# Optimization experiments

Measured on AMD Instinct MI355X. Metric: run time of the kernel, lower is better.

The kernel has to match this reference:

```python
import jax, jax.numpy as jnp
import numpy as np

N_TH1 = 30
LB = 1e-20
UB = 1e20
LB_EXP = -20.0
UB_EXP = 20.0


def make_directions(n_th1):
    # Reproduces the TF __init__ direction sampling on the sphere.
    n_th2 = 2 * (n_th1 - 1) + 1
    th1 = np.linspace(-np.pi / 2, np.pi / 2, n_th1)
    th2 = np.linspace(-np.pi, np.pi, n_th2)
    c1, s1 = np.cos(th1), np.sin(th1)
    c2, s2 = np.cos(th2), np.sin(th2)
    dx = np.outer(c1[1:-1], c2[:-1])          # [n_th1-2, n_th2-1]
    dy = np.outer(c1[1:-1], s2[:-1])
    dz = np.broadcast_to(s1[1:-1, None], dx.shape)
    mid = np.stack([dx, dy, dz], -1).reshape(-1, 3)
    poles = np.array([[c1[0] * c2[0], c1[0] * s2[0], s1[0]],
                      [c1[-1] * c2[0], c1[-1] * s2[0], s1[-1]]])
    return np.concatenate([mid, poles], 0).astype(np.float32)  # [D, 3]


def setup_inputs() -> dict:
    key = jax.random.key(0)
    k1, k2, k3 = jax.random.split(key, 3)
    vertices = jax.random.normal(k1, (8, 64, 32, 3), jnp.float32)
    # smoothness is a p-norm exponent; realistic range [2, 20]
    smoothness = 2.0 + 18.0 * jax.random.uniform(k2, (8, 64), jnp.float32)
    pointcloud = jax.random.normal(k3, (8, 2048, 3), jnp.float32)
    return {"vertices": vertices, "smoothness": smoothness, "pointcloud": pointcloud}


def _spt_forward(vertices, smoothness):
    dirs = jnp.asarray(make_directions(N_TH1))            # [D, 3]
    B, P = vertices.shape[0], vertices.shape[1]
    mean_v = jnp.mean(vertices, axis=2, keepdims=True)    # [B,P,1,3]
    local_v = vertices - mean_v                           # [B,P,V,3]

    # z = <v, x> for every vertex/direction pair -> [B,P,V,D]
    z = jnp.einsum('bpvc,dc->bpvd', local_v, dirs)
    zm = jnp.maximum(z, 0.0)
    p = smoothness[:, :, None, None]                      # [B,P,1,1]

    # dynamic rescaling k = 10^ceil(...) to keep zm^p in fp range
    zm_max = jnp.max(zm, axis=2, keepdims=True)           # [B,P,1,D]
    zm_log = jnp.log(zm_max) / jnp.log(10.0)              # = max over V of log10(zm)
    exponent = zm_log * p
    lk = jnp.where(exponent < LB_EXP, (-15.0 - exponent) / p, 0.0)
    k = 10.0 ** jnp.clip(jnp.ceil(lk), 0.0, UB_EXP)       # [B,P,1,D]
    k = jax.lax.stop_gradient(k)                          # ceil has zero grad anyway

    zm = zm * k
    pos = zm > 0
    # clip(zm^p, lb, ub) - (zm==0)*lb  ==  where(zm>0, clip(zm^p,lb,ub), 0)
    zm_p = jnp.where(pos, jnp.clip(jnp.where(pos, zm, 1.0) ** p, LB, UB), 0.0)
    sum_zm_p = jnp.sum(zm_p, axis=2, keepdims=True)       # [B,P,1,D]
    spos = sum_zm_p > 0
    h = jnp.where(spos, jnp.clip(jnp.where(spos, sum_zm_p, 1.0) ** (1.0 / p), LB, UB), LB)

    # dh/dz = clip((zm/h)^(p-1), lb, ub)
    ratio = zm / h                                        # [B,P,V,D]
    rpos = ratio > 0
    dhdz = jnp.where(rpos, jnp.clip(jnp.where(rpos, ratio, 1.0) ** (p - 1.0), LB, UB), LB)
    # dh/dx = dhdz^T @ vertices -> surface points
    dhdx = jnp.einsum('bpvd,bpvc->bpdc', dhdz, local_v)   # [B,P,D,3]
    surf = dhdx + mean_v                                  # broadcast [B,P,1,3]

    h_out = jnp.clip(h / k, -UB, UB)                      # [B,P,1,D]
    h_out = jnp.transpose(h_out, (0, 1, 3, 2))            # [B,P,D,1]
    local_dirs = jnp.broadcast_to(dirs[None, None], (B, P) + dirs.shape)
    direction_h = jnp.concatenate([local_dirs, h_out], axis=-1)  # [B,P,D,4]
    points = surf.reshape(B, -1, 3)                       # [B, P*D, 3]
    mean_out = mean_v.reshape(B, P, 3)
    return points, direction_h, mean_out, local_v


def reference(vertices, smoothness, pointcloud):
    points, direction_h, mean_out, local_v = _spt_forward(vertices, smoothness)
    B, P = vertices.shape[0], vertices.shape[1]
    # overlap / retraction loops are truncated in the source; placeholders
    overlap = jnp.zeros((B, P, 1), jnp.float32)
    retraction = jnp.zeros((B, P, 1), jnp.float32)
    return (points, direction_h, overlap, retraction, mean_out, local_v)
```

## Files before the change

### kernel.cpp

```cpp
#include <hip/hip_runtime.h>
#include <math.h>

#define NBP 512
#define VV 32
#define DD 1626
#define DSPAN 407

#define O_POINTS 0
#define O_DIRH   2497536
#define O_OVER   5827584
#define O_RETR   5828096
#define O_MEAN   5828608
#define O_LOCAL  5830144

#define L10_2 0.3010299956639812f
#define L2_10 3.321928094887362f
#define LH_MIN -66.43856189774725f

__device__ __forceinline__ float fexp2(float x) {
  return __builtin_amdgcn_exp2f(x);
}

__device__ __forceinline__ void make_dir_fast(int d, float& x, float& y, float& z) {
  if (d < 1624) {
    const int i1 = d / 58 + 1;
    const int i2 = d - (i1 - 1) * 58;
    const float STEP = 0.10833078115826873f;
    const float th1 = -1.5707963267948966f + (float)i1 * STEP;
    const float th2 = -3.14159265358979323846f + (float)i2 * STEP;
    const float s1 = __sinf(th1);
    const float c1 = __cosf(th1);
    const float s2 = __sinf(th2);
    const float c2 = __cosf(th2);
    x = c1 * c2; y = c1 * s2; z = s1;
  } else if (d == 1624) {
    x = -6.123234e-17f; y = -7.49880e-33f; z = -1.0f;
  } else {
    x = -6.123234e-17f; y = -7.49880e-33f; z = 1.0f;
  }
}

__global__ __launch_bounds__(256) void spt_kernel(
    const float* __restrict__ vertices,
    const float* __restrict__ smooth,
    float* __restrict__ out)
{
  const int bp  = blockIdx.x;
  const int bz  = blockIdx.y;
  const int tid = threadIdx.x;

  __shared__ __align__(16) float slvx[VV];
  __shared__ __align__(16) float slvy[VV];
  __shared__ __align__(16) float slvz[VV];

  const int dbase = bz * DSPAN;
  const int dend  = (DD - dbase) < DSPAN ? (DD - dbase) : DSPAN;

  const int v = tid & 31;
  const float* vp = vertices + bp * (VV * 3) + v * 3;
  const float vx = vp[0], vy = vp[1], vz = vp[2];
  float sx = vx, sy = vy, sz = vz;
#pragma unroll
  for (int m = 16; m >= 1; m >>= 1) {
    sx += __shfl_xor(sx, m);
    sy += __shfl_xor(sy, m);
    sz += __shfl_xor(sz, m);
  }
  const float mx = sx * (1.0f / 32.0f);
  const float my = sy * (1.0f / 32.0f);
  const float mz = sz * (1.0f / 32.0f);
  if (tid < VV) {
    slvx[tid] = vx - mx;
    slvy[tid] = vy - my;
    slvz[tid] = vz - mz;
  }
  __syncthreads();

  if (bz == 1) {
    if (tid < VV * 3) {
      const int vv = tid / 3, c = tid - vv * 3;
      const float val = (c == 0) ? slvx[vv] : ((c == 1) ? slvy[vv] : slvz[vv]);
      out[O_LOCAL + bp * (VV * 3) + tid] = val;
    }
    if (tid == 96) {
      out[O_MEAN + bp * 3 + 0] = mx;
      out[O_MEAN + bp * 3 + 1] = my;
      out[O_MEAN + bp * 3 + 2] = mz;
      out[O_OVER + bp] = 0.f;
      out[O_RETR + bp] = 0.f;
    }
  }

  const float p     = smooth[bp];
  const float inv_p = 1.0f / p;
  const float pm1   = p - 1.0f;
  const float plt   = p * L10_2;

  const float4* lvx4 = (const float4*)slvx;
  const float4* lvy4 = (const float4*)slvy;
  const float4* lvz4 = (const float4*)slvz;

  auto process = [&](int idx) {
    const int d = dbase + idx;
    float dx, dy, dz;
    make_dir_fast(d, dx, dy, dz);

    float zmax = 0.f;
#pragma unroll
    for (int j = 0; j < VV / 4; j++) {
      float4 X = lvx4[j], Y = lvy4[j], Z = lvz4[j];
      float z0 = fmaxf(fmaf(X.x, dx, fmaf(Y.x, dy, Z.x * dz)), 0.f);
      float z1 = fmaxf(fmaf(X.y, dx, fmaf(Y.y, dy, Z.y * dz)), 0.f);
      float z2 = fmaxf(fmaf(X.z, dx, fmaf(Y.z, dy, Z.z * dz)), 0.f);
      float z3 = fmaxf(fmaf(X.w, dx, fmaf(Y.w, dy, Z.w * dz)), 0.f);
      zmax = fmaxf(zmax, fmaxf(fmaxf(z0, z1), fmaxf(z2, z3)));
    }

    const float expo = __log2f(zmax) * plt;
    float kc = 0.f;
    if (expo < -20.f) {
      kc = fminf(fmaxf(ceilf((-15.f - expo) * inv_p), 0.f), 20.f);
    }
    const float kcl = kc * L2_10;
    const float A   = p * kcl;

    float ss0 = 0.f, ss1 = 0.f;
    float ax = 0.f, ay = 0.f, az = 0.f;
#pragma unroll
    for (int j = 0; j < VV / 4; j++) {
      float4 X = lvx4[j], Y = lvy4[j], Z = lvz4[j];
      float z0 = fmaxf(fmaf(X.x, dx, fmaf(Y.x, dy, Z.x * dz)), 0.f);
      float z1 = fmaxf(fmaf(X.y, dx, fmaf(Y.y, dy, Z.y * dz)), 0.f);
      float z2 = fmaxf(fmaf(X.z, dx, fmaf(Y.z, dy, Z.z * dz)), 0.f);
      float z3 = fmaxf(fmaf(X.w, dx, fmaf(Y.w, dy, Z.w * dz)), 0.f);
      float u0 = fexp2(fmaf(pm1, __log2f(z0), A));
      float u1 = fexp2(fmaf(pm1, __log2f(z1), A));
      float u2 = fexp2(fmaf(pm1, __log2f(z2), A));
      float u3 = fexp2(fmaf(pm1, __log2f(z3), A));
      ss0 = fmaf(u0, z0, ss0);  ss1 = fmaf(u1, z1, ss1);
      ss0 = fmaf(u2, z2, ss0);  ss1 = fmaf(u3, z3, ss1);
      ax = fmaf(u0, X.x, fmaf(u1, X.y, fmaf(u2, X.z, fmaf(u3, X.w, ax))));
      ay = fmaf(u0, Y.x, fmaf(u1, Y.y, fmaf(u2, Y.z, fmaf(u3, Y.w, ay))));
      az = fmaf(u0, Z.x, fmaf(u1, Z.y, fmaf(u2, Z.z, fmaf(u3, Z.w, az))));
    }
    const float ssum = ss0 + ss1;

    float lh = LH_MIN;
    float C2 = 0.f;
    if (ssum > 0.f) {
      lh = inv_p * __log2f(ssum);
      C2 = fexp2(-fmaf(pm1, lh, kcl));
    }

    const int pbase = bp * DD + d;
    out[O_POINTS + pbase * 3 + 0] = fmaf(C2, ax, mx);
    out[O_POINTS + pbase * 3 + 1] = fmaf(C2, ay, my);
    out[O_POINTS + pbase * 3 + 2] = fmaf(C2, az, mz);

    float4 dvh = make_float4(dx, dy, dz, fexp2(lh - kcl));
    ((float4*)(out + O_DIRH))[pbase] = dvh;
  };

  process(tid);
  if (tid + 256 < dend) process(256 + tid);
}

extern "C" void kernel_launch(void* const* d_in, const int* in_sizes, int n_in,
                              void* d_out, int out_size, void* d_ws, size_t ws_size,
                              hipStream_t stream) {
  const float* vertices = (const float*)d_in[0];
  const float* smooth   = (const float*)d_in[1];
  float* out = (float*)d_out;

  spt_kernel<<<dim3(NBP, 4), 256, 0, stream>>>(vertices, smooth, out);
}
```

Baseline: 77.70 us.

## Keep centered vertices in registers and halve the direction-split grid

Each thread now loads all 32 vertices into a 96-float register array and computes the mean itself. This removes the shared-memory staging, shuffles and __syncthreads, and every vertex operand comes from registers instead of LDS reads. The grid drops from 4 to 2 direction slices per (b,p), and each block loops over up to 4 direction chunks. The trade-off is much higher register pressure, which can cut occupancy, plus fewer blocks in flight (1024 vs 2048) and a serial tail in the last loop iteration.

New measurement: 77.39 us. No clear change (-0.4%).

```diff
diff --git a/kernel.cpp b/kernel.cpp
--- a/kernel.cpp
+++ b/kernel.cpp
@@ -4,7 +4,7 @@
 #define NBP 512
 #define VV 32
 #define DD 1626
-#define DSPAN 407
+#define DHALF 813
 
 #define O_POINTS 0
 #define O_DIRH   2497536
@@ -45,50 +45,52 @@
     const float* __restrict__ smooth,
     float* __restrict__ out)
 {
-  const int bp  = blockIdx.x;
-  const int bz  = blockIdx.y;
-  const int tid = threadIdx.x;
+  const int bp   = blockIdx.x;
+  const int half = blockIdx.y;
+  const int tid  = threadIdx.x;
 
-  __shared__ __align__(16) float slvx[VV];
-  __shared__ __align__(16) float slvy[VV];
-  __shared__ __align__(16) float slvz[VV];
+  const int dbase = half * DHALF;
 
-  const int dbase = bz * DSPAN;
-  const int dend  = (DD - dbase) < DSPAN ? (DD - dbase) : DSPAN;
+  float t[VV * 3];
+  {
+    const float4* vp4 = (const float4*)(vertices + bp * (VV * 3));
+#pragma unroll
+    for (int j = 0; j < 24; j++) {
+      float4 q = vp4[j];
+      t[j * 4 + 0] = q.x; t[j * 4 + 1] = q.y;
+      t[j * 4 + 2] = q.z; t[j * 4 + 3] = q.w;
+    }
+  }
 
-  const int v = tid & 31;
-  const float* vp = vertices + bp * (VV * 3) + v * 3;
-  const float vx = vp[0], vy = vp[1], vz = vp[2];
-  float sx = vx, sy = vy, sz = vz;
+  float mxa = 0.f, mxb = 0.f, mya = 0.f, myb = 0.f, mza = 0.f, mzb = 0.f;
 #pragma unroll
-  for (int m = 16; m >= 1; m >>= 1) {
-    sx += __shfl_xor(sx, m);
-    sy += __shfl_xor(sy, m);
-    sz += __shfl_xor(sz, m);
+  for (int i = 0; i < VV; i += 2) {
+    mxa += t[3 * i + 0];  mxb += t[3 * i + 3];
+    mya += t[3 * i + 1];  myb += t[3 * i + 4];
+    mza += t[3 * i + 2];  mzb += t[3 * i + 5];
   }
-  const float mx = sx * (1.0f / 32.0f);
-  const float my = sy * (1.0f / 32.0f);
-  const float mz = sz * (1.0f / 32.0f);
-  if (tid < VV) {
-    slvx[tid] = vx - mx;
-    slvy[tid] = vy - my;
-    slvz[tid] = vz - mz;
+  const float mx = (mxa + mxb) * (1.0f / 32.0f);
+  const float my = (mya + myb) * (1.0f / 32.0f);
+  const float mz = (mza + mzb) * (1.0f / 32.0f);
+
+#pragma unroll
+  for (int i = 0; i < VV; i++) {
+    t[3 * i + 0] -= mx;
+    t[3 * i + 1] -= my;
+    t[3 * i + 2] -= mz;
   }
-  __syncthreads();
 
-  if (bz == 1) {
-    if (tid < VV * 3) {
-      const int vv = tid / 3, c = tid - vv * 3;
-      const float val = (c == 0) ? slvx[vv] : ((c == 1) ? slvy[vv] : slvz[vv]);
-      out[O_LOCAL + bp * (VV * 3) + tid] = val;
+  if (half == 1 && tid == 0) {
+    float4* lp = (float4*)(out + O_LOCAL + bp * (VV * 3));
+#pragma unroll
+    for (int j = 0; j < 24; j++) {
+      lp[j] = make_float4(t[j * 4 + 0], t[j * 4 + 1], t[j * 4 + 2], t[j * 4 + 3]);
     }
-    if (tid == 96) {
-      out[O_MEAN + bp * 3 + 0] = mx;
-      out[O_MEAN + bp * 3 + 1] = my;
-      out[O_MEAN + bp * 3 + 2] = mz;
-      out[O_OVER + bp] = 0.f;
-      out[O_RETR + bp] = 0.f;
-    }
+    out[O_MEAN + bp * 3 + 0] = mx;
+    out[O_MEAN + bp * 3 + 1] = my;
+    out[O_MEAN + bp * 3 + 2] = mz;
+    out[O_OVER + bp] = 0.f;
+    out[O_RETR + bp] = 0.f;
   }
 
   const float p     = smooth[bp];
@@ -96,24 +98,19 @@
   const float pm1   = p - 1.0f;
   const float plt   = p * L10_2;
 
-  const float4* lvx4 = (const float4*)slvx;
-  const float4* lvy4 = (const float4*)slvy;
-  const float4* lvz4 = (const float4*)slvz;
-
-  auto process = [&](int idx) {
+#pragma unroll 1
+  for (int r = 0; r < 4; ++r) {
+    const int idx = r * 256 + tid;
+    if (idx >= DHALF) break;
     const int d = dbase + idx;
     float dx, dy, dz;
     make_dir_fast(d, dx, dy, dz);
 
     float zmax = 0.f;
 #pragma unroll
-    for (int j = 0; j < VV / 4; j++) {
-      float4 X = lvx4[j], Y = lvy4[j], Z = lvz4[j];
-      float z0 = fmaxf(fmaf(X.x, dx, fmaf(Y.x, dy, Z.x * dz)), 0.f);
-      float z1 = fmaxf(fmaf(X.y, dx, fmaf(Y.y, dy, Z.y * dz)), 0.f);
-      float z2 = fmaxf(fmaf(X.z, dx, fmaf(Y.z, dy, Z.z * dz)), 0.f);
-      float z3 = fmaxf(fmaf(X.w, dx, fmaf(Y.w, dy, Z.w * dz)), 0.f);
-      zmax = fmaxf(zmax, fmaxf(fmaxf(z0, z1), fmaxf(z2, z3)));
+    for (int i = 0; i < VV; i++) {
+      float zv = fmaxf(fmaf(t[3*i], dx, fmaf(t[3*i+1], dy, t[3*i+2] * dz)), 0.f);
+      zmax = fmaxf(zmax, zv);
     }
 
     const float expo = __log2f(zmax) * plt;
@@ -127,21 +124,16 @@
     float ss0 = 0.f, ss1 = 0.f;
     float ax = 0.f, ay = 0.f, az = 0.f;
 #pragma unroll
-    for (int j = 0; j < VV / 4; j++) {
-      float4 X = lvx4[j], Y = lvy4[j], Z = lvz4[j];
-      float z0 = fmaxf(fmaf(X.x, dx, fmaf(Y.x, dy, Z.x * dz)), 0.f);
-      float z1 = fmaxf(fmaf(X.y, dx, fmaf(Y.y, dy, Z.y * dz)), 0.f);
-      float z2 = fmaxf(fmaf(X.z, dx, fmaf(Y.z, dy, Z.z * dz)), 0.f);
-      float z3 = fmaxf(fmaf(X.w, dx, fmaf(Y.w, dy, Z.w * dz)), 0.f);
+    for (int i = 0; i < VV; i += 2) {
+      float z0 = fmaxf(fmaf(t[3*i+0], dx, fmaf(t[3*i+1], dy, t[3*i+2] * dz)), 0.f);
+      float z1 = fmaxf(fmaf(t[3*i+3], dx, fmaf(t[3*i+4], dy, t[3*i+5] * dz)), 0.f);
       float u0 = fexp2(fmaf(pm1, __log2f(z0), A));
       float u1 = fexp2(fmaf(pm1, __log2f(z1), A));
-      float u2 = fexp2(fmaf(pm1, __log2f(z2), A));
-      float u3 = fexp2(fmaf(pm1, __log2f(z3), A));
-      ss0 = fmaf(u0, z0, ss0);  ss1 = fmaf(u1, z1, ss1);
-      ss0 = fmaf(u2, z2, ss0);  ss1 = fmaf(u3, z3, ss1);
-      ax = fmaf(u0, X.x, fmaf(u1, X.y, fmaf(u2, X.z, fmaf(u3, X.w, ax))));
-      ay = fmaf(u0, Y.x, fmaf(u1, Y.y, fmaf(u2, Y.z, fmaf(u3, Y.w, ay))));
-      az = fmaf(u0, Z.x, fmaf(u1, Z.y, fmaf(u2, Z.z, fmaf(u3, Z.w, az))));
+      ss0 = fmaf(u0, z0, ss0);
+      ss1 = fmaf(u1, z1, ss1);
+      ax = fmaf(u0, t[3*i+0], fmaf(u1, t[3*i+3], ax));
+      ay = fmaf(u0, t[3*i+1], fmaf(u1, t[3*i+4], ay));
+      az = fmaf(u0, t[3*i+2], fmaf(u1, t[3*i+5], az));
     }
     const float ssum = ss0 + ss1;
 
@@ -159,10 +151,7 @@
 
     float4 dvh = make_float4(dx, dy, dz, fexp2(lh - kcl));
     ((float4*)(out + O_DIRH))[pbase] = dvh;
-  };
-
-  process(tid);
-  if (tid + 256 < dend) process(256 + tid);
+  }
 }
 
 extern "C" void kernel_launch(void* const* d_in, const int* in_sizes, int n_in,
@@ -172,5 +161,5 @@
   const float* smooth   = (const float*)d_in[1];
   float* out = (float*)d_out;
 
-  spt_kernel<<<dim3(NBP, 4), 256, 0, stream>>>(vertices, smooth, out);
+  spt_kernel<<<dim3(NBP, 2), 256, 0, stream>>>(vertices, smooth, out);
 }
```
